# Kernel optimization log

Hardware: AMD Instinct MI355X
Metric: run time of the kernel (lower is better)

Reference implementation:

```python
import jax, jax.numpy as jnp
import numpy as np

HID = 768
NSPLITS = 12
HEAD_RATIO = 2
H = NSPLITS // HEAD_RATIO          # 6 attention heads
D = HID // NSPLITS                 # 64 head size
AH = H * D                         # 384 all_head_size
KS = 9                             # conv kernel size
PAD = (KS - 1) // 2
B, S = 4, 1024


def setup_inputs() -> dict:
    key = jax.random.key(0)
    ks = jax.random.split(key, 16)
    std = 0.02
    inp = {
        "Q": jax.random.normal(ks[0], (B, S, HID), jnp.float32),
        "K": jax.random.normal(ks[1], (B, S, HID), jnp.float32),
        "V": jax.random.normal(ks[2], (B, S, HID), jnp.float32),
        "td": jax.random.uniform(ks[3], (B, S), jnp.float32),
        "mask": jax.random.randint(ks[4], (B, S), 0, 2, jnp.int32),
        # projection weights, applied as x @ W (in, out)
        "Wq": jax.random.normal(ks[5], (HID, AH), jnp.float32) * std,
        "Wk": jax.random.normal(ks[6], (HID, AH), jnp.float32) * std,
        "Wv": jax.random.normal(ks[7], (HID, AH), jnp.float32) * std,
        # separable conv: depthwise (HID, KS), pointwise (AH, HID), bias (AH,)
        "dw_w": jax.random.normal(ks[8], (HID, KS), jnp.float32) * std,
        "pw_w": jax.random.normal(ks[9], (AH, HID), jnp.float32) * std,
        "sep_b": jnp.zeros((AH,), jnp.float32),
        # conv_kernel_layer Linear(AH -> H*KS)
        "ck_W": jax.random.normal(ks[10], (AH, H * KS), jnp.float32) * std,
        "ck_b": jnp.zeros((H * KS,), jnp.float32),
        # conv_out_layer Linear(HID -> AH)
        "co_W": jax.random.normal(ks[11], (HID, AH), jnp.float32) * std,
        "co_b": jnp.zeros((AH,), jnp.float32),
        # gammas init to zeros as in torch module
        "gammas": jnp.zeros((H, 1, 1), jnp.float32),
    }
    return inp


def dist_func(scores, td, am, gammas):
    # scores: [B,H,S,S]; am: [B,1,1,S] bool key mask; entirely non-differentiable.
    s = scores.shape[-1]
    dt = scores.dtype
    amf = am.astype(dt)
    p = jax.nn.softmax(jnp.where(am, scores, -1e8), axis=-1) * amf
    distcum = jnp.cumsum(p, axis=-1)
    disttotal = jnp.sum(p, axis=-1, keepdims=True)
    # |j - i| position distance
    pos = jnp.abs(jnp.arange(s)[None, :] - jnp.arange(s)[:, None]).astype(dt)
    dist_scores = jnp.sqrt(jnp.clip((disttotal - distcum) * pos[None, None], 0.0, None))
    gamma = -jax.nn.softplus(gammas)[None]  # (1,H,1,1)
    total_effect = jnp.clip(jnp.exp(dist_scores * gamma), 1e-5, 1e5)
    # time-distance effect on strictly-lower-triangular positions
    tdn = td / jnp.maximum(jnp.linalg.norm(td, axis=-1, keepdims=True), 1e-12)
    td_scores = jnp.broadcast_to(tdn[:, None, None, :], scores.shape)
    td_sm = jax.nn.softmax(jnp.where(am, td_scores, -1e4), axis=-1)
    lower = jnp.tril(jnp.ones((s, s), dt), -1)  # (triu == 0)
    return jax.lax.stop_gradient(total_effect - td_sm * lower[None, None])


def reference(Q, K, V, td, mask, Wq, Wk, Wv, dw_w, pw_w, sep_b, ck_W, ck_b, co_W, co_b, gammas):
    b, s, hid = Q.shape
    mq = Q @ Wq  # (B,S,AH)
    mk = K @ Wk
    mv = V @ Wv
    # SeparableConv1D over sequence dim of K
    x = jnp.transpose(K, (0, 2, 1))  # (B,HID,S)
    dw = jax.lax.conv_general_dilated(
        x, dw_w[:, None, :], window_strides=(1,), padding=[(PAD, PAD)],
        feature_group_count=hid, dimension_numbers=("NCH", "OIH", "NCH"))
    pw = jnp.einsum("bcs,oc->bos", dw, pw_w) + sep_b[None, :, None]
    mkc = jnp.transpose(pw, (0, 2, 1))  # (B,S,AH)

    q = mq.reshape(b, s, H, D).transpose(0, 2, 1, 3)
    k = mk.reshape(b, s, H, D).transpose(0, 2, 1, 3)
    v = mv.reshape(b, s, H, D).transpose(0, 2, 1, 3)

    # dynamic span convolution
    conv_attn = mkc * mq                                   # (B,S,AH)
    ck = (conv_attn @ ck_W + ck_b).reshape(b, s, H, KS)
    ck = jax.nn.softmax(ck, axis=-1)                       # per-position kernel
    co = V @ co_W + co_b                                   # (B,S,AH)
    co_pad = jnp.pad(co, ((0, 0), (PAD, PAD), (0, 0)))
    idx = jnp.arange(s)[:, None] + jnp.arange(KS)[None, :]  # (S,KS)
    unf = co_pad[:, idx, :].reshape(b, s, KS, H, D)         # sliding window gather
    conv_out = jnp.einsum("bskhd,bshk->bshd", unf, ck)      # (B,S,H,D)

    # attention with distance decay
    scores = jnp.einsum("bhid,bhjd->bhij", q, k) / np.float32(np.sqrt(D))
    am = (mask[:, None, None, :] != 0)  # (B,1,1,S) key mask
    total_effect = dist_func(scores, td, am, gammas)
    scores = jnp.where(am, scores * total_effect, -1e8)
    probs = jax.nn.softmax(scores, axis=-1)
    ctx = jnp.einsum("bhij,bhjd->bhid", probs, v).transpose(0, 2, 1, 3)  # (B,S,H,D)

    out = jnp.concatenate([ctx, conv_out], axis=2).reshape(b, s, HEAD_RATIO * AH)
    return out
```

## Files before the change

kernel.cpp:

```cpp
#include <hip/hip_runtime.h>
#include <hip/hip_bf16.h>

#define HIDC 768
#define Hh   6
#define Dd   64
#define AHc  384
#define KSc  9
#define PADc 4
#define Bb   4
#define Ss   1024
#define MRr  (Bb * Ss)

typedef __attribute__((ext_vector_type(8))) __bf16 bf16x8;
typedef __attribute__((ext_vector_type(4))) float  f32x4;

__device__ __forceinline__ void split8(const float* p, bf16x8& hi, bf16x8& lo) {
    float4 x0 = *(const float4*)p;
    float4 x1 = *(const float4*)(p + 4);
    float xs[8] = {x0.x, x0.y, x0.z, x0.w, x1.x, x1.y, x1.z, x1.w};
#pragma unroll
    for (int e = 0; e < 8; ++e) {
        __bf16 hv = (__bf16)xs[e];
        hi[e] = hv;
        lo[e] = (__bf16)(xs[e] - (float)hv);
    }
}

__device__ __forceinline__ void split8r(const float* xs, bf16x8& hi, bf16x8& lo) {
#pragma unroll
    for (int e = 0; e < 8; ++e) {
        __bf16 hv = (__bf16)xs[e];
        hi[e] = hv;
        lo[e] = (__bf16)(xs[e] - (float)hv);
    }
}

__device__ __forceinline__ bf16x8 cvt8(const float* p) {
    float4 x0 = *(const float4*)p;
    float4 x1 = *(const float4*)(p + 4);
    float xs[8] = {x0.x, x0.y, x0.z, x0.w, x1.x, x1.y, x1.z, x1.w};
    bf16x8 h;
#pragma unroll
    for (int e = 0; e < 8; ++e) h[e] = (__bf16)xs[e];
    return h;
}

__global__ void k_depthwise(const float* __restrict__ Kin, const float* __restrict__ dww,
                            float* __restrict__ dwseq) {
    int idx = blockIdx.x * 256 + threadIdx.x;
    if (idx >= Bb * Ss * HIDC / 4) return;
    int c4 = idx % (HIDC / 4);
    int s  = (idx / (HIDC / 4)) % Ss;
    int b  = idx / ((HIDC / 4) * Ss);
    int c  = c4 * 4;
    float wv[4][KSc];
#pragma unroll
    for (int j = 0; j < 4; ++j)
#pragma unroll
        for (int k = 0; k < KSc; ++k) wv[j][k] = dww[(c + j) * KSc + k];
    float4 acc = {0.f, 0.f, 0.f, 0.f};
#pragma unroll
    for (int k = 0; k < KSc; ++k) {
        int sp = s + k - PADc;
        if (sp >= 0 && sp < Ss) {
            float4 v = *(const float4*)&Kin[(size_t)(b * Ss + sp) * HIDC + c];
            acc.x += v.x * wv[0][k]; acc.y += v.y * wv[1][k];
            acc.z += v.z * wv[2][k]; acc.w += v.w * wv[3][k];
        }
    }
    *(float4*)&dwseq[(size_t)idx * 4] = acc;
}

__global__ __launch_bounds__(256) void k_wsplit_t(const float* __restrict__ Wq, const float* __restrict__ Wk,
                                                  const float* __restrict__ Wv, const float* __restrict__ coW,
                                                  __bf16* __restrict__ Whi, __bf16* __restrict__ Wlo) {
    int z = blockIdx.z;
    const float* src = (z == 0) ? Wq : (z == 1) ? Wk : (z == 2) ? Wv : coW;
    int n0 = blockIdx.x * 64, k0 = blockIdx.y * 64;
    int tid = threadIdx.x;
    int r = tid >> 2, cq = tid & 3;
    __shared__ float tile[64][65];
#pragma unroll
    for (int e = 0; e < 4; ++e) {
        float4 v = *(const float4*)&src[(size_t)(k0 + r) * AHc + n0 + cq * 16 + e * 4];
        tile[r][cq * 16 + e * 4 + 0] = v.x;
        tile[r][cq * 16 + e * 4 + 1] = v.y;
        tile[r][cq * 16 + e * 4 + 2] = v.z;
        tile[r][cq * 16 + e * 4 + 3] = v.w;
    }
    __syncthreads();
    float x[16];
#pragma unroll
    for (int e = 0; e < 16; ++e) x[e] = tile[cq * 16 + e][r];
    bf16x8 h0, l0, h1, l1;
    split8r(x, h0, l0);
    split8r(x + 8, h1, l1);
    size_t dst = ((size_t)(z * AHc + n0 + r)) * HIDC + k0 + cq * 16;
    *(bf16x8*)(Whi + dst)     = h0;
    *(bf16x8*)(Whi + dst + 8) = h1;
    *(bf16x8*)(Wlo + dst)     = l0;
    *(bf16x8*)(Wlo + dst + 8) = l1;
}

__global__ void k_wsplit_c(const float* __restrict__ pww,
                           __bf16* __restrict__ Whi, __bf16* __restrict__ Wlo) {
    int idx = blockIdx.x * 256 + threadIdx.x;
    if (idx >= AHc * HIDC / 8) return;
    bf16x8 hi, lo;
    split8(pww + (size_t)idx * 8, hi, lo);
    size_t dst = (size_t)4 * AHc * HIDC + (size_t)idx * 8;
    *(bf16x8*)(Whi + dst) = hi;
    *(bf16x8*)(Wlo + dst) = lo;
}

__global__ void k_qkvsplit(const float* __restrict__ mq, const float* __restrict__ mk,
                           const float* __restrict__ mv,
                           __bf16* __restrict__ qh, __bf16* __restrict__ kh,
                           __bf16* __restrict__ kl, __bf16* __restrict__ vh) {
    const int n8 = MRr * AHc / 8;
    int idx = blockIdx.x * 256 + threadIdx.x;
    if (idx >= 3 * n8) return;
    int which = idx / n8, i8 = idx % n8;
    if (which == 0) {
        *(bf16x8*)(qh + (size_t)i8 * 8) = cvt8(mq + (size_t)i8 * 8);
    } else if (which == 1) {
        bf16x8 hi, lo;
        split8(mk + (size_t)i8 * 8, hi, lo);
        *(bf16x8*)(kh + (size_t)i8 * 8) = hi;
        *(bf16x8*)(kl + (size_t)i8 * 8) = lo;
    } else {
        *(bf16x8*)(vh + (size_t)i8 * 8) = cvt8(mv + (size_t)i8 * 8);
    }
}

__global__ void k_bias(const float* __restrict__ cob, const float* __restrict__ sepb,
                       float* __restrict__ biasb) {
    int idx = blockIdx.x * 256 + threadIdx.x;
    if (idx >= 5 * AHc) return;
    int z = idx / AHc, n = idx % AHc;
    biasb[idx] = (z == 3) ? cob[n] : (z == 4) ? sepb[n] : 0.f;
}

__global__ __launch_bounds__(256) void k_gemm5(
        const float* __restrict__ Q, const float* __restrict__ Kin,
        const float* __restrict__ V, const float* __restrict__ dwseq,
        const __bf16* __restrict__ Whi, const __bf16* __restrict__ Wlo,
        const float* __restrict__ biasb, float* __restrict__ Call) {
    __shared__ __attribute__((aligned(16))) __bf16 As_hi[128 * 40];
    __shared__ __attribute__((aligned(16))) __bf16 Bs_hi[128 * 40];
    __shared__ __attribute__((aligned(16))) __bf16 Bs_lo[128 * 40];

    int z = blockIdx.z;
    const float* Asrc = (z == 0) ? Q : (z == 1) ? Kin : (z <= 3) ? V : dwseq;
    int m0 = blockIdx.y * 128, n0 = blockIdx.x * 128;
    int tid = threadIdx.x;
    int wave = tid >> 6, lane = tid & 63, quad = lane >> 4, l15 = lane & 15;

    int sr = tid >> 1;
    int sk = (tid & 1) * 16;
    const float* Arow = Asrc + (size_t)(m0 + sr) * HIDC + sk;
    const __bf16* BhiRow = Whi + ((size_t)(z * AHc + n0 + sr)) * HIDC + sk;
    const __bf16* BloRow = Wlo + ((size_t)(z * AHc + n0 + sr)) * HIDC + sk;

    f32x4 acc[4][4] = {};

    for (int k0 = 0; k0 < HIDC; k0 += 32) {
        const float* ap = Arow + k0;
        *(bf16x8*)&As_hi[sr * 40 + sk]     = cvt8(ap);
        *(bf16x8*)&As_hi[sr * 40 + sk + 8] = cvt8(ap + 8);
        {
            const __bf16* bh = BhiRow + k0;
            const __bf16* bl = BloRow + k0;
            *(bf16x8*)&Bs_hi[sr * 40 + sk]     = *(const bf16x8*)bh;
            *(bf16x8*)&Bs_hi[sr * 40 + sk + 8] = *(const bf16x8*)(bh + 8);
            *(bf16x8*)&Bs_lo[sr * 40 + sk]     = *(const bf16x8*)bl;
            *(bf16x8*)&Bs_lo[sr * 40 + sk + 8] = *(const bf16x8*)(bl + 8);
        }
        __syncthreads();

        int mrow = (wave >> 1) * 64 + l15;
        int nrow = (wave & 1) * 64 + l15;
        bf16x8 ah[4], bh[4], bl[4];
#pragma unroll
        for (int mt = 0; mt < 4; ++mt)
            ah[mt] = *(bf16x8*)&As_hi[(mrow + mt * 16) * 40 + quad * 8];
#pragma unroll
        for (int nt = 0; nt < 4; ++nt) {
            bh[nt] = *(bf16x8*)&Bs_hi[(nrow + nt * 16) * 40 + quad * 8];
            bl[nt] = *(bf16x8*)&Bs_lo[(nrow + nt * 16) * 40 + quad * 8];
        }
#pragma unroll
        for (int mt = 0; mt < 4; ++mt)
#pragma unroll
            for (int nt = 0; nt < 4; ++nt) {
                acc[mt][nt] = __builtin_amdgcn_mfma_f32_16x16x32_bf16(ah[mt], bh[nt], acc[mt][nt], 0, 0, 0);
                acc[mt][nt] = __builtin_amdgcn_mfma_f32_16x16x32_bf16(ah[mt], bl[nt], acc[mt][nt], 0, 0, 0);
            }
        __syncthreads();
    }

    float* Cz = Call + (size_t)z * MRr * AHc;
    const float* bz = biasb + z * AHc;
#pragma unroll
    for (int nt = 0; nt < 4; ++nt) {
        int n = n0 + (wave & 1) * 64 + nt * 16 + l15;
        float bias = bz[n];
#pragma unroll
        for (int mt = 0; mt < 4; ++mt) {
#pragma unroll
            for (int r = 0; r < 4; ++r) {
                int m = m0 + (wave >> 1) * 64 + mt * 16 + quad * 4 + r;
                Cz[(size_t)m * AHc + n] = acc[mt][nt][r] + bias;
            }
        }
    }
}

__global__ __launch_bounds__(64) void k_ck(const float* __restrict__ mkc, const float* __restrict__ mq,
                                           const float* __restrict__ ckW, const float* __restrict__ ckb,
                                           float* __restrict__ ck_sm) {
    int row = blockIdx.x;
    int tid = threadIdx.x;
    __shared__ float ca[AHc];
    __shared__ float ckv[Hh * KSc];
    for (int o = tid; o < AHc; o += 64)
        ca[o] = mkc[row * AHc + o] * mq[row * AHc + o];
    __syncthreads();
    if (tid < Hh * KSc) {
        float acc = ckb[tid];
        for (int o = 0; o < AHc; ++o)
            acc += ca[o] * ckW[o * (Hh * KSc) + tid];
        ckv[tid] = acc;
    }
    __syncthreads();
    if (tid < Hh) {
        float m = -3e38f;
#pragma unroll
        for (int k = 0; k < KSc; ++k) m = fmaxf(m, ckv[tid * KSc + k]);
        float e[KSc];
        float s = 0.f;
#pragma unroll
        for (int k = 0; k < KSc; ++k) { e[k] = expf(ckv[tid * KSc + k] - m); s += e[k]; }
        float inv = 1.f / s;
#pragma unroll
        for (int k = 0; k < KSc; ++k) ck_sm[(row * Hh + tid) * KSc + k] = e[k] * inv;
    }
}

__global__ void k_convout(const float* __restrict__ co, const float* __restrict__ ck_sm,
                          float* __restrict__ out) {
    int idx = blockIdx.x * 256 + threadIdx.x;
    if (idx >= Bb * Ss * AHc / 4) return;
    int d4 = idx & 15;
    int h  = (idx >> 4) % Hh;
    int s  = (idx / (AHc / 4)) % Ss;
    int b  = idx / ((AHc / 4) * Ss);
    int row = b * Ss + s;
    const float* ck = ck_sm + (size_t)(row * Hh + h) * KSc;
    float4 acc = {0.f, 0.f, 0.f, 0.f};
#pragma unroll
    for (int k = 0; k < KSc; ++k) {
        int sp = s + k - PADc;
        if (sp >= 0 && sp < Ss) {
            float4 v = *(const float4*)&co[(size_t)(b * Ss + sp) * AHc + h * Dd + d4 * 4];
            float wv = ck[k];
            acc.x += wv * v.x; acc.y += wv * v.y; acc.z += wv * v.z; acc.w += wv * v.w;
        }
    }
    *(float4*)&out[(size_t)row * (2 * AHc) + AHc + h * Dd + d4 * 4] = acc;
}

__global__ __launch_bounds__(256) void k_td(const float* __restrict__ td, const int* __restrict__ mask,
                                            float* __restrict__ td_sm) {
    int b = blockIdx.x;
    int tid = threadIdx.x;
    __shared__ float red[256];
    __shared__ float tv[Ss];
    float ls = 0.f;
    for (int j = tid; j < Ss; j += 256) {
        float v = td[b * Ss + j];
        tv[j] = v;
        ls += v * v;
    }
    red[tid] = ls; __syncthreads();
    for (int s = 128; s > 0; s >>= 1) { if (tid < s) red[tid] += red[tid + s]; __syncthreads(); }
    float norm = fmaxf(sqrtf(red[0]), 1e-12f);
    __syncthreads();
    float lm = -3e38f;
    for (int j = tid; j < Ss; j += 256) {
        float v = mask[b * Ss + j] ? tv[j] / norm : -1e4f;
        tv[j] = v;
        lm = fmaxf(lm, v);
    }
    red[tid] = lm; __syncthreads();
    for (int s = 128; s > 0; s >>= 1) { if (tid < s) red[tid] = fmaxf(red[tid], red[tid + s]); __syncthreads(); }
    float m = red[0]; __syncthreads();
    float lsum = 0.f;
    for (int j = tid; j < Ss; j += 256) {
        float e = expf(tv[j] - m);
        tv[j] = e;
        lsum += e;
    }
    red[tid] = lsum; __syncthreads();
    for (int s = 128; s > 0; s >>= 1) { if (tid < s) red[tid] += red[tid + s]; __syncthreads(); }
    float inv = 1.f / red[0];
    __syncthreads();
    for (int j = tid; j < Ss; j += 256)
        td_sm[b * Ss + j] = tv[j] * inv;
}

__device__ __forceinline__ int sidx(int m, int j) {
    return m * 1024 + (j & ~15) + ((j ^ (j >> 6) ^ m) & 15);
}

__global__ __launch_bounds__(256) void k_attn(const __bf16* __restrict__ qh,
                                              const __bf16* __restrict__ kh, const __bf16* __restrict__ kl,
                                              const __bf16* __restrict__ vh,
                                              const int* __restrict__ mask,
                                              const float* __restrict__ td_sm, const float* __restrict__ gammas,
                                              float* __restrict__ out) {
    __shared__ float sc[16 * 1024];
    int i0 = blockIdx.x * 16;
    int h = blockIdx.y % Hh, b = blockIdx.y / Hh;
    int tid = threadIdx.x;
    int w = tid >> 6, lane = tid & 63, quad = lane >> 4, l15 = lane & 15;
    int jw = w * 256;

    bf16x8 a_hi[2];
    {
        size_t qoff = (size_t)(b * Ss + i0 + l15) * AHc + h * Dd + quad * 8;
        a_hi[0] = *(const bf16x8*)(qh + qoff);
        a_hi[1] = *(const bf16x8*)(qh + qoff + 32);
    }
#pragma unroll 2
    for (int t = 0; t < 16; ++t) {
        int jt = jw + t * 16;
        size_t koff = (size_t)(b * Ss + jt + l15) * AHc + h * Dd + quad * 8;
        f32x4 acc = {0.f, 0.f, 0.f, 0.f};
#pragma unroll
        for (int kc = 0; kc < 2; ++kc) {
            bf16x8 khv = *(const bf16x8*)(kh + koff + kc * 32);
            bf16x8 klv = *(const bf16x8*)(kl + koff + kc * 32);
            acc = __builtin_amdgcn_mfma_f32_16x16x32_bf16(a_hi[kc], khv, acc, 0, 0, 0);
            acc = __builtin_amdgcn_mfma_f32_16x16x32_bf16(a_hi[kc], klv, acc, 0, 0, 0);
        }
#pragma unroll
        for (int r = 0; r < 4; ++r)
            sc[sidx(quad * 4 + r, jt + l15)] = acc[r] * 0.125f;
    }
    __syncthreads();

    const int* mrow = mask + b * Ss;
    const float* tdrow = td_sm + b * Ss;
    float gamma = -log1pf(expf(gammas[h]));
    int jb = lane << 4;
    int marr[16];
    {
        const int4* mp = (const int4*)(mrow + jb);
#pragma unroll
        for (int k = 0; k < 4; ++k) ((int4*)marr)[k] = mp[k];
    }
    float tdv[16];
    {
        const float4* tp = (const float4*)(tdrow + jb);
#pragma unroll
        for (int k = 0; k < 4; ++k) ((float4*)tdv)[k] = tp[k];
    }

#pragma unroll
    for (int r4 = 0; r4 < 4; ++r4) {
        int m = w * 4 + r4;
        int i = i0 + m;
        float s[16], p[16];
#pragma unroll
        for (int jj = 0; jj < 16; ++jj) s[jj] = sc[sidx(m, jb + jj)];
        float mx = -1e30f;
#pragma unroll
        for (int jj = 0; jj < 16; ++jj) mx = fmaxf(mx, marr[jj] ? s[jj] : -1e30f);
        mx = fmaxf(mx, __shfl_xor(mx, 1));  mx = fmaxf(mx, __shfl_xor(mx, 2));
        mx = fmaxf(mx, __shfl_xor(mx, 4));  mx = fmaxf(mx, __shfl_xor(mx, 8));
        mx = fmaxf(mx, __shfl_xor(mx, 16)); mx = fmaxf(mx, __shfl_xor(mx, 32));
#pragma unroll
        for (int jj = 0; jj < 16; ++jj) p[jj] = marr[jj] ? __expf(s[jj] - mx) : 0.f;
#pragma unroll
        for (int jj = 1; jj < 16; ++jj) p[jj] += p[jj - 1];
        float t = p[15];
        float incl = t;
#pragma unroll
        for (int dlt = 1; dlt < 64; dlt <<= 1) {
            float v = __shfl_up(incl, dlt);
            if (lane >= dlt) incl += v;
        }
        float off = incl - t;
        float tot = __shfl(incl, 63);
        float inv = 1.f / fmaxf(tot, 1e-30f);
        float mx2 = -1e30f;
#pragma unroll
        for (int jj = 0; jj < 16; ++jj) {
            int j = jb + jj;
            float cum = p[jj] + off;
            float pos = fabsf((float)(j - i));
            float ds = sqrtf(fmaxf((tot - cum) * inv * pos, 0.f));
            float te = fminf(fmaxf(__expf(ds * gamma), 1e-5f), 1e5f);
            float mult = te - ((j < i) ? tdv[jj] : 0.f);
            float s2 = marr[jj] ? s[jj] * mult : -1e8f;
            s[jj] = s2;
            mx2 = fmaxf(mx2, s2);
        }
        mx2 = fmaxf(mx2, __shfl_xor(mx2, 1));  mx2 = fmaxf(mx2, __shfl_xor(mx2, 2));
        mx2 = fmaxf(mx2, __shfl_xor(mx2, 4));  mx2 = fmaxf(mx2, __shfl_xor(mx2, 8));
        mx2 = fmaxf(mx2, __shfl_xor(mx2, 16)); mx2 = fmaxf(mx2, __shfl_xor(mx2, 32));
        float sm = 0.f;
#pragma unroll
        for (int jj = 0; jj < 16; ++jj) { s[jj] = __expf(s[jj] - mx2); sm += s[jj]; }
        sm += __shfl_xor(sm, 1);  sm += __shfl_xor(sm, 2);
        sm += __shfl_xor(sm, 4);  sm += __shfl_xor(sm, 8);
        sm += __shfl_xor(sm, 16); sm += __shfl_xor(sm, 32);
        float inv2 = 1.f / sm;
#pragma unroll
        for (int jj = 0; jj < 16; ++jj) sc[sidx(m, jb + jj)] = s[jj] * inv2;
    }
    __syncthreads();

    f32x4 oacc[4] = {};
    const __bf16* vbase = vh + (size_t)b * Ss * AHc + h * Dd;
#pragma unroll 2
    for (int kc = 0; kc < 8; ++kc) {
        int j0 = jw + kc * 32 + quad * 8;
        float x[8];
#pragma unroll
        for (int jj = 0; jj < 8; ++jj) x[jj] = sc[sidx(l15, j0 + jj)];
        bf16x8 p_hi, p_lo;
        split8r(x, p_hi, p_lo);
#pragma unroll
        for (int nt = 0; nt < 4; ++nt) {
            int d = nt * 16 + l15;
            bf16x8 vv;
#pragma unroll
            for (int e = 0; e < 8; ++e) vv[e] = vbase[(size_t)(j0 + e) * AHc + d];
            oacc[nt] = __builtin_amdgcn_mfma_f32_16x16x32_bf16(p_hi, vv, oacc[nt], 0, 0, 0);
            oacc[nt] = __builtin_amdgcn_mfma_f32_16x16x32_bf16(p_lo, vv, oacc[nt], 0, 0, 0);
        }
    }
    __syncthreads();
#pragma unroll
    for (int nt = 0; nt < 4; ++nt)
#pragma unroll
        for (int r = 0; r < 4; ++r)
            sc[w * 1024 + (quad * 4 + r) * 64 + nt * 16 + l15] = oacc[nt][r];
    __syncthreads();
#pragma unroll
    for (int e = 0; e < 4; ++e) {
        int idx = e * 256 + tid;
        int m = idx >> 6, dd = idx & 63;
        float v = sc[idx] + sc[1024 + idx] + sc[2048 + idx] + sc[3072 + idx];
        out[(size_t)(b * Ss + i0 + m) * (2 * AHc) + h * Dd + dd] = v;
    }
}

extern "C" void kernel_launch(void* const* d_in, const int* in_sizes, int n_in,
                              void* d_out, int out_size, void* d_ws, size_t ws_size,
                              hipStream_t stream) {
    const float* Q    = (const float*)d_in[0];
    const float* Kin  = (const float*)d_in[1];
    const float* V    = (const float*)d_in[2];
    const float* td   = (const float*)d_in[3];
    const int*   mask = (const int*)d_in[4];
    const float* Wq   = (const float*)d_in[5];
    const float* Wk   = (const float*)d_in[6];
    const float* Wv   = (const float*)d_in[7];
    const float* dww  = (const float*)d_in[8];
    const float* pww  = (const float*)d_in[9];
    const float* sepb = (const float*)d_in[10];
    const float* ckW  = (const float*)d_in[11];
    const float* ckb  = (const float*)d_in[12];
    const float* coW  = (const float*)d_in[13];
    const float* cob  = (const float*)d_in[14];
    const float* gam  = (const float*)d_in[15];
    float* out = (float*)d_out;
    float* ws = (float*)d_ws;

    float* mq    = ws;
    float* mk    = mq    + (size_t)MRr * AHc;
    float* mv    = mk    + (size_t)MRr * AHc;
    float* co    = mv    + (size_t)MRr * AHc;
    float* mkc   = co    + (size_t)MRr * AHc;
    float* dwseq = mkc   + (size_t)MRr * AHc;
    float* cksm  = dwseq + (size_t)MRr * HIDC;
    float* tdsm  = cksm  + (size_t)MRr * Hh * KSc;
    float* biasb = tdsm  + (size_t)Bb * Ss;

    __bf16* Whi = (__bf16*)d_out;
    __bf16* Wlo = Whi + (size_t)5 * AHc * HIDC;
    __bf16* qh = (__bf16*)dwseq;
    __bf16* kh = qh + (size_t)MRr * AHc;
    __bf16* kl = kh + (size_t)MRr * AHc;
    __bf16* vh = kl + (size_t)MRr * AHc;

    dim3 gt(AHc / 64, HIDC / 64, 4);
    k_wsplit_t<<<gt, 256, 0, stream>>>(Wq, Wk, Wv, coW, Whi, Wlo);
    k_wsplit_c<<<(AHc * HIDC / 8 + 255) / 256, 256, 0, stream>>>(pww, Whi, Wlo);
    k_depthwise<<<(MRr * HIDC / 4 + 255) / 256, 256, 0, stream>>>(Kin, dww, dwseq);
    k_bias<<<(5 * AHc + 255) / 256, 256, 0, stream>>>(cob, sepb, biasb);

    dim3 gg(AHc / 128, MRr / 128, 5);
    k_gemm5<<<gg, 256, 0, stream>>>(Q, Kin, V, dwseq, Whi, Wlo, biasb, mq);

    k_qkvsplit<<<(3 * MRr * AHc / 8 + 255) / 256, 256, 0, stream>>>(mq, mk, mv, qh, kh, kl, vh);
    k_ck<<<MRr, 64, 0, stream>>>(mkc, mq, ckW, ckb, cksm);
    k_convout<<<(MRr * AHc / 4 + 255) / 256, 256, 0, stream>>>(co, cksm, out);
    k_td<<<Bb, 256, 0, stream>>>(td, mask, tdsm);

    dim3 ga(Ss / 16, Bb * Hh);
    k_attn<<<ga, 256, 0, stream>>>(qh, kh, kl, vh, mask, tdsm, gam, out);
}
```

Measured before the change: 303.7 us.

## Transpose V to head-major bf16 and widen attention blocks to 512 threads

A new kernel writes V as a per-head transposed bf16 layout, so the PV MFMA operand becomes one vector load instead of eight strided scalar loads. The attention kernel now runs 8 waves per block, each covering 128 keys, and the final reduction sums over 8 partial outputs. The score-tile swizzle is changed so that softmax and PV reads and writes use 16-byte vector shared-memory accesses. This adds a transpose kernel launch and a wider cross-wave reduction in exchange for less global and shared-memory access overhead.

Result: no change. 301.0 us (-0.9%).

```diff
diff --git a/kernel.cpp b/kernel.cpp
--- a/kernel.cpp
+++ b/kernel.cpp
@@ -114,23 +114,48 @@
 }
 
 __global__ void k_qkvsplit(const float* __restrict__ mq, const float* __restrict__ mk,
-                           const float* __restrict__ mv,
                            __bf16* __restrict__ qh, __bf16* __restrict__ kh,
-                           __bf16* __restrict__ kl, __bf16* __restrict__ vh) {
+                           __bf16* __restrict__ kl) {
     const int n8 = MRr * AHc / 8;
     int idx = blockIdx.x * 256 + threadIdx.x;
-    if (idx >= 3 * n8) return;
+    if (idx >= 2 * n8) return;
     int which = idx / n8, i8 = idx % n8;
     if (which == 0) {
         *(bf16x8*)(qh + (size_t)i8 * 8) = cvt8(mq + (size_t)i8 * 8);
-    } else if (which == 1) {
+    } else {
         bf16x8 hi, lo;
         split8(mk + (size_t)i8 * 8, hi, lo);
         *(bf16x8*)(kh + (size_t)i8 * 8) = hi;
         *(bf16x8*)(kl + (size_t)i8 * 8) = lo;
-    } else {
-        *(bf16x8*)(vh + (size_t)i8 * 8) = cvt8(mv + (size_t)i8 * 8);
-    }
+    }
+}
+
+__global__ __launch_bounds__(256) void k_vtrans(const float* __restrict__ mv,
+                                                __bf16* __restrict__ vt) {
+    int s0 = blockIdx.x * 64;
+    int h = blockIdx.y % Hh, b = blockIdx.y / Hh;
+    int tid = threadIdx.x;
+    int r = tid >> 2, cq = tid & 3;
+    __shared__ float tile[64][65];
+    const float* src = mv + (size_t)(b * Ss + s0 + r) * AHc + h * Dd + cq * 16;
+#pragma unroll
+    for (int e = 0; e < 4; ++e) {
+        float4 v = *(const float4*)(src + e * 4);
+        tile[r][cq * 16 + e * 4 + 0] = v.x;
+        tile[r][cq * 16 + e * 4 + 1] = v.y;
+        tile[r][cq * 16 + e * 4 + 2] = v.z;
+        tile[r][cq * 16 + e * 4 + 3] = v.w;
+    }
+    __syncthreads();
+    bf16x8 o0, o1;
+#pragma unroll
+    for (int e = 0; e < 8; ++e) {
+        o0[e] = (__bf16)tile[cq * 16 + e][r];
+        o1[e] = (__bf16)tile[cq * 16 + 8 + e][r];
+    }
+    __bf16* dst = vt + ((size_t)((b * Hh + h) * Dd + r)) * Ss + s0 + cq * 16;
+    *(bf16x8*)dst       = o0;
+    *(bf16x8*)(dst + 8) = o1;
 }
 
 __global__ void k_bias(const float* __restrict__ cob, const float* __restrict__ sepb,
@@ -309,13 +334,13 @@
         td_sm[b * Ss + j] = tv[j] * inv;
 }
 
-__device__ __forceinline__ int sidx(int m, int j) {
-    return m * 1024 + (j & ~15) + ((j ^ (j >> 6) ^ m) & 15);
-}
-
-__global__ __launch_bounds__(256) void k_attn(const __bf16* __restrict__ qh,
+__device__ __forceinline__ int scix(int m, int j) {
+    return m * 1024 + (j ^ (((m ^ (j >> 6)) & 7) << 2));
+}
+
+__global__ __launch_bounds__(512) void k_attn(const __bf16* __restrict__ qh,
                                               const __bf16* __restrict__ kh, const __bf16* __restrict__ kl,
-                                              const __bf16* __restrict__ vh,
+                                              const __bf16* __restrict__ vt,
                                               const int* __restrict__ mask,
                                               const float* __restrict__ td_sm, const float* __restrict__ gammas,
                                               float* __restrict__ out) {
@@ -324,7 +349,7 @@
     int h = blockIdx.y % Hh, b = blockIdx.y / Hh;
     int tid = threadIdx.x;
     int w = tid >> 6, lane = tid & 63, quad = lane >> 4, l15 = lane & 15;
-    int jw = w * 256;
+    int jw = w * 128;
 
     bf16x8 a_hi[2];
     {
@@ -333,7 +358,7 @@
         a_hi[1] = *(const bf16x8*)(qh + qoff + 32);
     }
 #pragma unroll 2
-    for (int t = 0; t < 16; ++t) {
+    for (int t = 0; t < 8; ++t) {
         int jt = jw + t * 16;
         size_t koff = (size_t)(b * Ss + jt + l15) * AHc + h * Dd + quad * 8;
         f32x4 acc = {0.f, 0.f, 0.f, 0.f};
@@ -346,7 +371,7 @@
         }
 #pragma unroll
         for (int r = 0; r < 4; ++r)
-            sc[sidx(quad * 4 + r, jt + l15)] = acc[r] * 0.125f;
+            sc[scix(quad * 4 + r, jt + l15)] = acc[r] * 0.125f;
     }
     __syncthreads();
 
@@ -354,13 +379,13 @@
     const float* tdrow = td_sm + b * Ss;
     float gamma = -log1pf(expf(gammas[h]));
     int jb = lane << 4;
-    int marr[16];
+    __attribute__((aligned(16))) int marr[16];
     {
         const int4* mp = (const int4*)(mrow + jb);
 #pragma unroll
         for (int k = 0; k < 4; ++k) ((int4*)marr)[k] = mp[k];
     }
-    float tdv[16];
+    __attribute__((aligned(16))) float tdv[16];
     {
         const float4* tp = (const float4*)(tdrow + jb);
 #pragma unroll
@@ -368,12 +393,14 @@
     }
 
 #pragma unroll
-    for (int r4 = 0; r4 < 4; ++r4) {
-        int m = w * 4 + r4;
+    for (int r4 = 0; r4 < 2; ++r4) {
+        int m = w * 2 + r4;
         int i = i0 + m;
-        float s[16], p[16];
-#pragma unroll
-        for (int jj = 0; jj < 16; ++jj) s[jj] = sc[sidx(m, jb + jj)];
+        __attribute__((aligned(16))) float s[16];
+        float p[16];
+#pragma unroll
+        for (int g = 0; g < 4; ++g)
+            *(f32x4*)(s + 4 * g) = *(const f32x4*)&sc[scix(m, jb + 4 * g)];
         float mx = -1e30f;
 #pragma unroll
         for (int jj = 0; jj < 16; ++jj) mx = fmaxf(mx, marr[jj] ? s[jj] : -1e30f);
@@ -418,26 +445,27 @@
         sm += __shfl_xor(sm, 16); sm += __shfl_xor(sm, 32);
         float inv2 = 1.f / sm;
 #pragma unroll
-        for (int jj = 0; jj < 16; ++jj) sc[sidx(m, jb + jj)] = s[jj] * inv2;
+        for (int jj = 0; jj < 16; ++jj) s[jj] *= inv2;
+#pragma unroll
+        for (int g = 0; g < 4; ++g)
+            *(f32x4*)&sc[scix(m, jb + 4 * g)] = *(const f32x4*)(s + 4 * g);
     }
     __syncthreads();
 
     f32x4 oacc[4] = {};
-    const __bf16* vbase = vh + (size_t)b * Ss * AHc + h * Dd;
-#pragma unroll 2
-    for (int kc = 0; kc < 8; ++kc) {
+    const __bf16* vtb = vt + (size_t)(b * Hh + h) * Dd * Ss;
+#pragma unroll
+    for (int kc = 0; kc < 4; ++kc) {
         int j0 = jw + kc * 32 + quad * 8;
-        float x[8];
-#pragma unroll
-        for (int jj = 0; jj < 8; ++jj) x[jj] = sc[sidx(l15, j0 + jj)];
+        __attribute__((aligned(16))) float x[8];
+        *(f32x4*)x       = *(const f32x4*)&sc[scix(l15, j0)];
+        *(f32x4*)(x + 4) = *(const f32x4*)&sc[scix(l15, j0 + 4)];
         bf16x8 p_hi, p_lo;
         split8r(x, p_hi, p_lo);
 #pragma unroll
         for (int nt = 0; nt < 4; ++nt) {
             int d = nt * 16 + l15;
-            bf16x8 vv;
-#pragma unroll
-            for (int e = 0; e < 8; ++e) vv[e] = vbase[(size_t)(j0 + e) * AHc + d];
+            bf16x8 vv = *(const bf16x8*)(vtb + (size_t)d * Ss + j0);
             oacc[nt] = __builtin_amdgcn_mfma_f32_16x16x32_bf16(p_hi, vv, oacc[nt], 0, 0, 0);
             oacc[nt] = __builtin_amdgcn_mfma_f32_16x16x32_bf16(p_lo, vv, oacc[nt], 0, 0, 0);
         }
@@ -450,10 +478,12 @@
             sc[w * 1024 + (quad * 4 + r) * 64 + nt * 16 + l15] = oacc[nt][r];
     __syncthreads();
 #pragma unroll
-    for (int e = 0; e < 4; ++e) {
-        int idx = e * 256 + tid;
+    for (int e = 0; e < 2; ++e) {
+        int idx = e * 512 + tid;
         int m = idx >> 6, dd = idx & 63;
-        float v = sc[idx] + sc[1024 + idx] + sc[2048 + idx] + sc[3072 + idx];
+        float v = 0.f;
+#pragma unroll
+        for (int ww = 0; ww < 8; ++ww) v += sc[ww * 1024 + idx];
         out[(size_t)(b * Ss + i0 + m) * (2 * AHc) + h * Dd + dd] = v;
     }
 }
@@ -495,7 +525,7 @@
     __bf16* qh = (__bf16*)dwseq;
     __bf16* kh = qh + (size_t)MRr * AHc;
     __bf16* kl = kh + (size_t)MRr * AHc;
-    __bf16* vh = kl + (size_t)MRr * AHc;
+    __bf16* vt = kl + (size_t)MRr * AHc;
 
     dim3 gt(AHc / 64, HIDC / 64, 4);
     k_wsplit_t<<<gt, 256, 0, stream>>>(Wq, Wk, Wv, coW, Whi, Wlo);
@@ -506,11 +536,12 @@
     dim3 gg(AHc / 128, MRr / 128, 5);
     k_gemm5<<<gg, 256, 0, stream>>>(Q, Kin, V, dwseq, Whi, Wlo, biasb, mq);
 
-    k_qkvsplit<<<(3 * MRr * AHc / 8 + 255) / 256, 256, 0, stream>>>(mq, mk, mv, qh, kh, kl, vh);
+    k_qkvsplit<<<(2 * MRr * AHc / 8 + 255) / 256, 256, 0, stream>>>(mq, mk, qh, kh, kl);
+    k_vtrans<<<dim3(Ss / 64, Bb * Hh), 256, 0, stream>>>(mv, vt);
     k_ck<<<MRr, 64, 0, stream>>>(mkc, mq, ckW, ckb, cksm);
     k_convout<<<(MRr * AHc / 4 + 255) / 256, 256, 0, stream>>>(co, cksm, out);
     k_td<<<Bb, 256, 0, stream>>>(td, mask, tdsm);
 
     dim3 ga(Ss / 16, Bb * Hh);
-    k_attn<<<ga, 256, 0, stream>>>(qh, kh, kl, vh, mask, tdsm, gam, out);
-}
+    k_attn<<<ga, 512, 0, stream>>>(qh, kh, kl, vt, mask, tdsm, gam, out);
+}
```
